# Performance work log

Measured on AMD Instinct MI355X. Metric: run time of the kernel, lower is better.

Reference implementation:

```python
import jax, jax.numpy as jnp
import numpy as np

B, N, K, C, NH = 2, 16384, 16, 256, 4
HD = C // NH  # head_dim = 64


def knn_gather(feat, idx):
    # feat: [B, N, D], idx: [B, N, K] -> [B, N, K, D]
    b, n, k = idx.shape
    d = feat.shape[-1]
    flat = jnp.take_along_axis(feat, idx.reshape(b, n * k)[..., None], axis=1)
    return flat.reshape(b, n, k, d)


def setup_inputs() -> dict:
    key = jax.random.key(0)
    ks = jax.random.split(key, 16)
    s_c = 1.0 / np.sqrt(C)
    s_4 = 1.0 / np.sqrt(4.0)
    s_hd = 1.0 / np.sqrt(HD)
    return {
        'h': jax.random.normal(ks[0], (B, N, C), jnp.float32),
        'P': jax.random.normal(ks[1], (B, 3, N), jnp.float32),
        'idx': jax.random.randint(ks[2], (B, N, K), 0, N),
        'Wq': jax.random.normal(ks[3], (C, C), jnp.float32) * s_c,
        'Wk': jax.random.normal(ks[4], (C, C), jnp.float32) * s_c,
        'Wv': jax.random.normal(ks[5], (C, C), jnp.float32) * s_c,
        'Wp1': jax.random.normal(ks[6], (4, C), jnp.float32) * s_4,
        'bp1': jnp.zeros((C,), jnp.float32),
        'Wp2': jax.random.normal(ks[7], (C, C), jnp.float32) * s_c,
        'bp2': jnp.zeros((C,), jnp.float32),
        'Wa1': jax.random.normal(ks[8], (HD, HD), jnp.float32) * s_hd,
        'ba1': jnp.zeros((HD,), jnp.float32),
        'Wa2': jax.random.normal(ks[9], (HD, 1), jnp.float32) * s_hd,
        'ba2': jnp.zeros((1,), jnp.float32),
        'Wo': jax.random.normal(ks[10], (C, C), jnp.float32) * s_c,
        'bo': jnp.zeros((C,), jnp.float32),
    }


def reference(h, P, idx, Wq, Wk, Wv, Wp1, bp1, Wp2, bp2, Wa1, ba1, Wa2, ba2, Wo, bo):
    b, n, c = h.shape
    P_t = jnp.swapaxes(P, 1, 2)                       # [B, N, 3]
    P_nbr = knn_gather(P_t, idx)                      # [B, N, K, 3]
    rel_pos = P_nbr - P_t[:, :, None, :]              # [B, N, K, 3]
    dist = jnp.linalg.norm(rel_pos, axis=-1, keepdims=True)
    geom = jnp.concatenate([rel_pos, dist], axis=-1)  # [B, N, K, 4]
    pe = jax.nn.relu(geom @ Wp1 + bp1) @ Wp2 + bp2    # [B, N, K, C]
    pe = pe.reshape(b, n, K, NH, HD)

    Q = (h @ Wq).reshape(b, n, 1, NH, HD)
    K_nbr = knn_gather(h @ Wk, idx).reshape(b, n, K, NH, HD)
    V_nbr = knn_gather(h @ Wv, idx).reshape(b, n, K, NH, HD)

    relation = Q - K_nbr + pe                          # [B, N, K, NH, HD]
    logits = jax.nn.relu(relation @ Wa1 + ba1) @ Wa2 + ba2  # [B, N, K, NH, 1]
    attn = jax.nn.softmax(logits, axis=2)              # softmax over K
    agg = jnp.sum(attn * (V_nbr + pe), axis=2)         # [B, N, NH, HD]
    agg = agg.reshape(b, n, c)
    return agg @ Wo + bo
```

## Files before the change

### kernel.cpp

```cpp
#include <hip/hip_runtime.h>
#include <hip/hip_bf16.h>

#define BB 2
#define NN 16384
#define KK 16
#define CC 256
#define NHH 4
#define HDD 64
#define BN (BB*NN)
#define HP 260

typedef __attribute__((ext_vector_type(8))) short short8;
typedef __attribute__((ext_vector_type(4))) short s4;
typedef __attribute__((ext_vector_type(4))) float f32x4;

__device__ __forceinline__ float bf2f(unsigned short u) {
    union { unsigned u32; float f; } x; x.u32 = ((unsigned)u) << 16; return x.f;
}
__device__ __forceinline__ unsigned short f2bf(float f) {
    union { float f; unsigned u; } x; x.f = f;
    unsigned r = x.u + 0x7FFFu + ((x.u >> 16) & 1u);
    return (unsigned short)(r >> 16);
}
__device__ __forceinline__ short8 ld8_lds(const unsigned short* p) {
    s4 lo = *(const s4*)(p);
    s4 hi = *(const s4*)(p + 4);
    short8 r;
    r[0] = lo[0]; r[1] = lo[1]; r[2] = lo[2]; r[3] = lo[3];
    r[4] = hi[0]; r[5] = hi[1]; r[6] = hi[2]; r[7] = hi[3];
    return r;
}

__global__ __launch_bounds__(256) void prep_kernel(
    const float* __restrict__ Wq, const float* __restrict__ Wk,
    const float* __restrict__ Wv, const float* __restrict__ Wp2,
    const float* __restrict__ Wo, const float* __restrict__ Wa1,
    const float* __restrict__ bp2, const float* __restrict__ ba1,
    const float* __restrict__ Wp1,
    unsigned short* WqaT, unsigned short* WkaT, unsigned short* WvT,
    unsigned short* WpeaT, unsigned short* Wp2T, unsigned short* WoT,
    float* b_u, unsigned short* Wp1aT)
{
    const int z = blockIdx.y;
    const int t = threadIdx.x;
    if (z < 3) {
        const float* W = (z == 0) ? Wq : (z == 1) ? Wk : Wp2;
        unsigned short* out = (z == 0) ? WqaT : (z == 1) ? WkaT : WpeaT;
        const int k = blockIdx.x;
        __shared__ float wrow[CC];
        __shared__ float a1[HDD * HDD];
        wrow[t] = W[k * CC + t];
        for (int i = t; i < HDD * HDD; i += 256) a1[i] = Wa1[i];
        __syncthreads();
        const int c = t;
        const int h0 = c & ~63;
        const int cl = c & 63;
        float s = 0.f;
        #pragma unroll 8
        for (int j = 0; j < HDD; ++j) s += wrow[h0 + j] * a1[j * HDD + cl];
        out[c * CC + k] = f2bf(s);
    } else if (z < 6) {
        const float* W = (z == 3) ? Wv : (z == 4) ? Wp2 : Wo;
        unsigned short* out = (z == 3) ? WvT : (z == 4) ? Wp2T : WoT;
        const int k = blockIdx.x;
        out[t * CC + k] = f2bf(W[k * CC + t]);
    } else {
        if (blockIdx.x == 0) {
            __shared__ float a1[HDD * HDD];
            for (int i = t; i < HDD * HDD; i += 256) a1[i] = Wa1[i];
            __syncthreads();
            const int c = t;
            const int h0 = c & ~63;
            const int cl = c & 63;
            float s = ba1[cl];
            #pragma unroll 8
            for (int j = 0; j < HDD; ++j) s += bp2[h0 + j] * a1[j * HDD + cl];
            b_u[c] = s;
        } else if (blockIdx.x == 1) {
            const int c = t;
            #pragma unroll
            for (int j = 0; j < 8; ++j)
                Wp1aT[c * 8 + j] = (j < 4) ? f2bf(Wp1[j * CC + c]) : (unsigned short)0;
        }
    }
}

__global__ __launch_bounds__(256) void h2bf_kernel(const float* __restrict__ h,
                                                   unsigned short* __restrict__ hbf)
{
    const int i = blockIdx.x * blockDim.x + threadIdx.x;
    const float4 v = ((const float4*)h)[i];
    ushort4 o;
    o.x = f2bf(v.x); o.y = f2bf(v.y); o.z = f2bf(v.z); o.w = f2bf(v.w);
    ((ushort4*)hbf)[i] = o;
}

template<bool FINAL>
__global__ __launch_bounds__(256) void gemm64_kernel(
    const unsigned short* __restrict__ A,
    const unsigned short* __restrict__ BT0, const unsigned short* __restrict__ BT1,
    const unsigned short* __restrict__ BT2,
    unsigned short* D0, unsigned short* D1, unsigned short* D2,
    float* Dout, const float* __restrict__ bias)
{
    const int m0 = blockIdx.x * 64;
    const unsigned short* BT;
    unsigned short* Dst = nullptr;
    if (!FINAL) {
        const int z = blockIdx.y;
        BT  = (z == 0) ? BT0 : (z == 1) ? BT1 : BT2;
        Dst = (z == 0) ? D0  : (z == 1) ? D1  : D2;
    } else {
        BT = BT0;
    }

    __shared__ __align__(16) unsigned short As[64 * 264];
    const int t = threadIdx.x;
    #pragma unroll
    for (int i = 0; i < 8; ++i) {
        const int flat = i * 2048 + t * 8;
        const int r = flat >> 8, c = flat & 255;
        short8 v = *(const short8*)(A + (size_t)(m0 + r) * CC + c);
        *(short8*)(&As[r * 264 + c]) = v;
    }
    __syncthreads();

    const int lane = t & 63, w = t >> 6;
    const int lr = lane & 15, lg = lane >> 4;

    f32x4 acc[4][4];
    #pragma unroll
    for (int mi = 0; mi < 4; ++mi)
        #pragma unroll
        for (int ni = 0; ni < 4; ++ni) acc[mi][ni] = (f32x4){0.f, 0.f, 0.f, 0.f};

    #pragma unroll
    for (int kk = 0; kk < 8; ++kk) {
        const int ko = kk * 32 + lg * 8;
        short8 a[4];
        #pragma unroll
        for (int mi = 0; mi < 4; ++mi)
            a[mi] = *(const short8*)(&As[(mi * 16 + lr) * 264 + ko]);
        #pragma unroll
        for (int ni = 0; ni < 4; ++ni) {
            const int col = w * 64 + ni * 16 + lr;
            short8 b = *(const short8*)(BT + (size_t)col * CC + ko);
            #pragma unroll
            for (int mi = 0; mi < 4; ++mi)
                acc[mi][ni] = __builtin_amdgcn_mfma_f32_16x16x32_bf16(a[mi], b, acc[mi][ni], 0, 0, 0);
        }
    }

    #pragma unroll
    for (int mi = 0; mi < 4; ++mi) {
        #pragma unroll
        for (int ni = 0; ni < 4; ++ni) {
            const int col = w * 64 + ni * 16 + lr;
            #pragma unroll
            for (int reg = 0; reg < 4; ++reg) {
                const int row = m0 + mi * 16 + lg * 4 + reg;
                const float v = acc[mi][ni][reg];
                if (FINAL) Dout[(size_t)row * CC + col] = v + bias[col];
                else       Dst[(size_t)row * CC + col] = f2bf(v);
            }
        }
    }
}

__global__ __launch_bounds__(256, 4) void fused_attn_kernel(
    const float* __restrict__ P, const int* __restrict__ idx,
    const unsigned short* __restrict__ Wp1aT, const float* __restrict__ bp1,
    const float* __restrict__ Wa2, const float* __restrict__ bp2,
    const unsigned short* __restrict__ QAbf, const unsigned short* __restrict__ KAbf,
    const unsigned short* __restrict__ Vbf,  const unsigned short* __restrict__ WpeaT,
    const unsigned short* __restrict__ Wp2T, const float* __restrict__ b_u,
    unsigned short* __restrict__ aggbf)
{
    const int pt0 = blockIdx.x * 4;
    const int b = pt0 >> 14;
    const int n0 = pt0 & (NN - 1);
    const int t = threadIdx.x;
    const int lane = t & 63, w = t >> 6;
    const int lr = lane & 15, lg = lane >> 4;

    __shared__ int nbrL[64];
    __shared__ __align__(16) unsigned short geomP[64 * 8];
    __shared__ __align__(16) unsigned short hidL[64 * HP];
    __shared__ __align__(16) unsigned short attnA[16 * 72];
    __shared__ unsigned short vbarL[16 * 72];

    const short8 zero8 = {0, 0, 0, 0, 0, 0, 0, 0};

    float qab[4][4];
    float wa2v[4], bp1v[4];
    #pragma unroll
    for (int ni = 0; ni < 4; ++ni) {
        const int c = w * 64 + ni * 16 + lr;
        wa2v[ni] = Wa2[ni * 16 + lr];
        bp1v[ni] = bp1[c];
        const float bu = b_u[c];
        #pragma unroll
        for (int mi = 0; mi < 4; ++mi)
            qab[mi][ni] = bf2f(QAbf[(size_t)(pt0 + mi) * CC + c]) + bu;
    }

    for (int i = t; i < 576; i += 256) ((unsigned*)attnA)[i] = 0;
    if (t < 64) {
        const int g = t >> 4, k = t & 15;
        const int nb = idx[(size_t)(pt0 + g) * KK + k];
        nbrL[t] = nb;
        const float* Pb = P + (size_t)b * 3 * NN;
        const int nc = n0 + g;
        const float rx = Pb[nb] - Pb[nc];
        const float ry = Pb[NN + nb] - Pb[NN + nc];
        const float rz = Pb[2 * NN + nb] - Pb[2 * NN + nc];
        const float d = sqrtf(rx * rx + ry * ry + rz * rz);
        short8 gp = {(short)f2bf(rx), (short)f2bf(ry), (short)f2bf(rz), (short)f2bf(d),
                     0, 0, 0, 0};
        *(short8*)(&geomP[t * 8]) = gp;
    }
    __syncthreads();

    {
        short8 bb[4];
        #pragma unroll
        for (int ni = 0; ni < 4; ++ni) {
            const int col = w * 64 + ni * 16 + lr;
            bb[ni] = (lg == 0) ? *(const short8*)(Wp1aT + col * 8) : zero8;
        }
        #pragma unroll
        for (int mi = 0; mi < 4; ++mi) {
            short8 ag = (lg == 0) ? *(const short8*)(&geomP[(mi * 16 + lr) * 8]) : zero8;
            #pragma unroll
            for (int ni = 0; ni < 4; ++ni) {
                f32x4 ah = (f32x4){bp1v[ni], bp1v[ni], bp1v[ni], bp1v[ni]};
                ah = __builtin_amdgcn_mfma_f32_16x16x32_bf16(ag, bb[ni], ah, 0, 0, 0);
                const int col = w * 64 + ni * 16 + lr;
                #pragma unroll
                for (int reg = 0; reg < 4; ++reg)
                    hidL[(mi * 16 + lg * 4 + reg) * HP + col] = f2bf(fmaxf(ah[reg], 0.f));
            }
        }
    }
    __syncthreads();

    f32x4 acc[4][4];
    #pragma unroll
    for (int mi = 0; mi < 4; ++mi)
        #pragma unroll
        for (int ni = 0; ni < 4; ++ni) {
            const float v = qab[mi][ni];
            acc[mi][ni] = (f32x4){v, v, v, v};
        }

    #pragma unroll
    for (int kk = 0; kk < 8; ++kk) {
        const int ko = kk * 32 + lg * 8;
        short8 a[4];
        #pragma unroll
        for (int mi = 0; mi < 4; ++mi)
            a[mi] = ld8_lds(&hidL[(mi * 16 + lr) * HP + ko]);
        #pragma unroll
        for (int ni = 0; ni < 4; ++ni) {
            const int col = w * 64 + ni * 16 + lr;
            short8 bfr = *(const short8*)(WpeaT + (size_t)col * CC + ko);
            #pragma unroll
            for (int mi = 0; mi < 4; ++mi)
                acc[mi][ni] = __builtin_amdgcn_mfma_f32_16x16x32_bf16(a[mi], bfr, acc[mi][ni], 0, 0, 0);
        }
    }

    #pragma unroll
    for (int mi = 0; mi < 4; ++mi) {
        unsigned short ka[4][4];
        #pragma unroll
        for (int reg = 0; reg < 4; ++reg) {
            const int r = mi * 16 + lg * 4 + reg;
            const size_t base = ((size_t)b * NN + nbrL[r]) * CC;
            #pragma unroll
            for (int ni = 0; ni < 4; ++ni)
                ka[reg][ni] = KAbf[base + w * 64 + ni * 16 + lr];
        }
        float pl[4];
        #pragma unroll
        for (int reg = 0; reg < 4; ++reg) {
            float s = 0.f;
            #pragma unroll
            for (int ni = 0; ni < 4; ++ni) {
                const float u = acc[mi][ni][reg] - bf2f(ka[reg][ni]);
                s += fmaxf(u, 0.f) * wa2v[ni];
            }
            s += __shfl_xor(s, 1);
            s += __shfl_xor(s, 2);
            s += __shfl_xor(s, 4);
            s += __shfl_xor(s, 8);
            pl[reg] = s;
        }
        float m = fmaxf(fmaxf(pl[0], pl[1]), fmaxf(pl[2], pl[3]));
        m = fmaxf(m, __shfl_xor(m, 16));
        m = fmaxf(m, __shfl_xor(m, 32));
        float e[4], s = 0.f;
        #pragma unroll
        for (int reg = 0; reg < 4; ++reg) { e[reg] = __expf(pl[reg] - m); s += e[reg]; }
        s += __shfl_xor(s, 16);
        s += __shfl_xor(s, 32);
        const float inv = 1.f / s;
        if (lr == 0) {
            #pragma unroll
            for (int reg = 0; reg < 4; ++reg)
                attnA[(mi * 4 + w) * 72 + mi * 16 + lg * 4 + reg] = f2bf(e[reg] * inv);
        }
    }
    __syncthreads();

    unsigned short vv[4][16];
    #pragma unroll
    for (int i = 0; i < 4; ++i) {
        const int gh = w * 4 + i;
        const int g = gh >> 2, hh = gh & 3;
        #pragma unroll
        for (int k = 0; k < 16; ++k) {
            const int r = g * 16 + k;
            vv[i][k] = Vbf[((size_t)b * NN + nbrL[r]) * CC + hh * 64 + lane];
        }
    }

    #pragma unroll
    for (int ni = 0; ni < 4; ++ni) {
        const int colAbs = w * 64 + ni * 16 + lr;
        f32x4 ab = (f32x4){0.f, 0.f, 0.f, 0.f};
        #pragma unroll
        for (int kk = 0; kk < 2; ++kk) {
            short8 aa = ld8_lds(&attnA[lr * 72 + kk * 32 + lg * 8]);
            short8 hb;
            #pragma unroll
            for (int j = 0; j < 8; ++j)
                hb[j] = (short)hidL[(kk * 32 + lg * 8 + j) * HP + colAbs];
            ab = __builtin_amdgcn_mfma_f32_16x16x32_bf16(aa, hb, ab, 0, 0, 0);
        }
        #pragma unroll
        for (int reg = 0; reg < 4; ++reg)
            hidL[(lg * 4 + reg) * HP + colAbs] = f2bf(ab[reg]);
    }

    {
        #pragma unroll
        for (int i = 0; i < 4; ++i) {
            const int gh = w * 4 + i;
            const int g = gh >> 2;
            float s = 0.f;
            #pragma unroll
            for (int k = 0; k < 16; ++k)
                s += bf2f(attnA[gh * 72 + g * 16 + k]) * bf2f(vv[i][k]);
            vbarL[gh * 72 + lane] = f2bf(s);
        }
    }
    __syncthreads();

    f32x4 acc2[4];
    #pragma unroll
    for (int ni = 0; ni < 4; ++ni) acc2[ni] = (f32x4){0.f, 0.f, 0.f, 0.f};
    #pragma unroll
    for (int kk = 0; kk < 8; ++kk) {
        const int ko = kk * 32 + lg * 8;
        short8 a = ld8_lds(&hidL[lr * HP + ko]);
        #pragma unroll
        for (int ni = 0; ni < 4; ++ni) {
            const int col = w * 64 + ni * 16 + lr;
            short8 bfr = *(const short8*)(Wp2T + (size_t)col * CC + ko);
            acc2[ni] = __builtin_amdgcn_mfma_f32_16x16x32_bf16(a, bfr, acc2[ni], 0, 0, 0);
        }
    }
    #pragma unroll
    for (int ni = 0; ni < 4; ++ni) {
        const int cl = ni * 16 + lr;
        const int c = w * 64 + cl;
        float pv;
        if      (w == 0) pv = acc2[ni][0];
        else if (w == 1) pv = acc2[ni][1];
        else if (w == 2) pv = acc2[ni][2];
        else             pv = acc2[ni][3];
        const float v = pv + bf2f(vbarL[(lg * 4 + w) * 72 + cl]) + bp2[c];
        aggbf[(size_t)(pt0 + lg) * CC + c] = f2bf(v);
    }
}

extern "C" void kernel_launch(void* const* d_in, const int* in_sizes, int n_in,
                              void* d_out, int out_size, void* d_ws, size_t ws_size,
                              hipStream_t stream)
{
    const float* h   = (const float*)d_in[0];
    const float* P   = (const float*)d_in[1];
    const int*   idx = (const int*)d_in[2];
    const float* Wq  = (const float*)d_in[3];
    const float* Wk  = (const float*)d_in[4];
    const float* Wv  = (const float*)d_in[5];
    const float* Wp1 = (const float*)d_in[6];
    const float* bp1 = (const float*)d_in[7];
    const float* Wp2 = (const float*)d_in[8];
    const float* bp2 = (const float*)d_in[9];
    const float* Wa1 = (const float*)d_in[10];
    const float* ba1 = (const float*)d_in[11];
    const float* Wa2 = (const float*)d_in[12];
    const float* Wo  = (const float*)d_in[14];
    const float* bo  = (const float*)d_in[15];

    char* ws = (char*)d_ws;
    const size_t MB16 = 16777216;
    unsigned short* WqaT  = (unsigned short*)(ws + 0);
    unsigned short* WkaT  = (unsigned short*)(ws + 131072);
    unsigned short* WvT   = (unsigned short*)(ws + 262144);
    unsigned short* WpeaT = (unsigned short*)(ws + 393216);
    unsigned short* Wp2T  = (unsigned short*)(ws + 524288);
    unsigned short* WoT   = (unsigned short*)(ws + 655360);
    float*          b_u   = (float*)(ws + 786432);
    unsigned short* Wp1aT = (unsigned short*)(ws + 787456);
    const size_t base = 1 << 20;
    unsigned short* hbf   = (unsigned short*)(ws + base + 0 * MB16);
    unsigned short* QAbf  = (unsigned short*)(ws + base + 1 * MB16);
    unsigned short* KAbf  = (unsigned short*)(ws + base + 2 * MB16);
    unsigned short* Vbf   = (unsigned short*)(ws + base + 3 * MB16);
    unsigned short* aggbf = (unsigned short*)(ws + base + 4 * MB16);
    if (ws_size < base + 5 * MB16) return;

    prep_kernel<<<dim3(256, 7), 256, 0, stream>>>(Wq, Wk, Wv, Wp2, Wo, Wa1, bp2, ba1, Wp1,
                                                  WqaT, WkaT, WvT, WpeaT, Wp2T, WoT,
                                                  b_u, Wp1aT);
    h2bf_kernel<<<BN * CC / 4 / 256, 256, 0, stream>>>(h, hbf);
    gemm64_kernel<false><<<dim3(BN / 64, 3), 256, 0, stream>>>(
        hbf, WqaT, WkaT, WvT, QAbf, KAbf, Vbf, nullptr, nullptr);
    fused_attn_kernel<<<BN / 4, 256, 0, stream>>>(P, idx, Wp1aT, bp1, Wa2, bp2,
                                                  QAbf, KAbf, Vbf, WpeaT, Wp2T, b_u, aggbf);
    gemm64_kernel<true><<<dim3(BN / 64, 1), 256, 0, stream>>>(
        aggbf, WoT, nullptr, nullptr, nullptr, nullptr, nullptr, (float*)d_out, bo);
}
```

Before: 395.8 us.

## Fuse bf16 conversion into QKV GEMM, interleave K/V rows, fold bias into Q

The separate h-to-bf16 kernel is removed, and the QKV GEMM now reads fp32 h directly and converts it while staging into LDS. K and V outputs are written interleaved into a single 512-wide row buffer, so each gathered neighbor's K and V values sit in the same row and can share cache lines. The b_u bias add moves from the attention kernel into the Q GEMM epilogue. Together these remove one launch and a full bf16 write/read round trip, and should improve gather locality. The cost is that every z-slice of the GEMM now reads fp32 h, doubling A-load bytes per block, and Q is rounded to bf16 after the bias add.

```diff
diff --git a/kernel.cpp b/kernel.cpp
--- a/kernel.cpp
+++ b/kernel.cpp
@@ -9,6 +9,7 @@
 #define HDD 64
 #define BN (BB*NN)
 #define HP 260
+#define KVP 512
 
 typedef __attribute__((ext_vector_type(8))) short short8;
 typedef __attribute__((ext_vector_type(4))) short s4;
@@ -85,31 +86,20 @@
     }
 }
 
-__global__ __launch_bounds__(256) void h2bf_kernel(const float* __restrict__ h,
-                                                   unsigned short* __restrict__ hbf)
-{
-    const int i = blockIdx.x * blockDim.x + threadIdx.x;
-    const float4 v = ((const float4*)h)[i];
-    ushort4 o;
-    o.x = f2bf(v.x); o.y = f2bf(v.y); o.z = f2bf(v.z); o.w = f2bf(v.w);
-    ((ushort4*)hbf)[i] = o;
-}
-
-template<bool FINAL>
+template<bool FINAL, bool AF32>
 __global__ __launch_bounds__(256) void gemm64_kernel(
-    const unsigned short* __restrict__ A,
+    const void* __restrict__ Asrc,
     const unsigned short* __restrict__ BT0, const unsigned short* __restrict__ BT1,
     const unsigned short* __restrict__ BT2,
-    unsigned short* D0, unsigned short* D1, unsigned short* D2,
+    unsigned short* QA, unsigned short* KV,
     float* Dout, const float* __restrict__ bias)
 {
     const int m0 = blockIdx.x * 64;
     const unsigned short* BT;
-    unsigned short* Dst = nullptr;
+    int z = 0;
     if (!FINAL) {
-        const int z = blockIdx.y;
-        BT  = (z == 0) ? BT0 : (z == 1) ? BT1 : BT2;
-        Dst = (z == 0) ? D0  : (z == 1) ? D1  : D2;
+        z = blockIdx.y;
+        BT = (z == 0) ? BT0 : (z == 1) ? BT1 : BT2;
     } else {
         BT = BT0;
     }
@@ -120,8 +110,20 @@
     for (int i = 0; i < 8; ++i) {
         const int flat = i * 2048 + t * 8;
         const int r = flat >> 8, c = flat & 255;
-        short8 v = *(const short8*)(A + (size_t)(m0 + r) * CC + c);
-        *(short8*)(&As[r * 264 + c]) = v;
+        if (AF32) {
+            const float* Af = (const float*)Asrc;
+            const float4 v0 = *(const float4*)(Af + (size_t)(m0 + r) * CC + c);
+            const float4 v1 = *(const float4*)(Af + (size_t)(m0 + r) * CC + c + 4);
+            short8 v;
+            v[0] = (short)f2bf(v0.x); v[1] = (short)f2bf(v0.y);
+            v[2] = (short)f2bf(v0.z); v[3] = (short)f2bf(v0.w);
+            v[4] = (short)f2bf(v1.x); v[5] = (short)f2bf(v1.y);
+            v[6] = (short)f2bf(v1.z); v[7] = (short)f2bf(v1.w);
+            *(short8*)(&As[r * 264 + c]) = v;
+        } else {
+            short8 v = *(const short8*)((const unsigned short*)Asrc + (size_t)(m0 + r) * CC + c);
+            *(short8*)(&As[r * 264 + c]) = v;
+        }
     }
     __syncthreads();
 
@@ -156,12 +158,18 @@
         #pragma unroll
         for (int ni = 0; ni < 4; ++ni) {
             const int col = w * 64 + ni * 16 + lr;
+            const float bc = (FINAL || z == 0) ? bias[col] : 0.f;
             #pragma unroll
             for (int reg = 0; reg < 4; ++reg) {
                 const int row = m0 + mi * 16 + lg * 4 + reg;
                 const float v = acc[mi][ni][reg];
-                if (FINAL) Dout[(size_t)row * CC + col] = v + bias[col];
-                else       Dst[(size_t)row * CC + col] = f2bf(v);
+                if (FINAL) {
+                    Dout[(size_t)row * CC + col] = v + bias[col];
+                } else if (z == 0) {
+                    QA[(size_t)row * CC + col] = f2bf(v + bc);
+                } else {
+                    KV[(size_t)row * KVP + (z == 1 ? 0 : 256) + col] = f2bf(v);
+                }
             }
         }
     }
@@ -171,9 +179,8 @@
     const float* __restrict__ P, const int* __restrict__ idx,
     const unsigned short* __restrict__ Wp1aT, const float* __restrict__ bp1,
     const float* __restrict__ Wa2, const float* __restrict__ bp2,
-    const unsigned short* __restrict__ QAbf, const unsigned short* __restrict__ KAbf,
-    const unsigned short* __restrict__ Vbf,  const unsigned short* __restrict__ WpeaT,
-    const unsigned short* __restrict__ Wp2T, const float* __restrict__ b_u,
+    const unsigned short* __restrict__ QAbf, const unsigned short* __restrict__ KVbf,
+    const unsigned short* __restrict__ WpeaT, const unsigned short* __restrict__ Wp2T,
     unsigned short* __restrict__ aggbf)
 {
     const int pt0 = blockIdx.x * 4;
@@ -198,10 +205,9 @@
         const int c = w * 64 + ni * 16 + lr;
         wa2v[ni] = Wa2[ni * 16 + lr];
         bp1v[ni] = bp1[c];
-        const float bu = b_u[c];
         #pragma unroll
         for (int mi = 0; mi < 4; ++mi)
-            qab[mi][ni] = bf2f(QAbf[(size_t)(pt0 + mi) * CC + c]) + bu;
+            qab[mi][ni] = bf2f(QAbf[(size_t)(pt0 + mi) * CC + c]);
     }
 
     for (int i = t; i < 576; i += 256) ((unsigned*)attnA)[i] = 0;
@@ -276,10 +282,10 @@
         #pragma unroll
         for (int reg = 0; reg < 4; ++reg) {
             const int r = mi * 16 + lg * 4 + reg;
-            const size_t base = ((size_t)b * NN + nbrL[r]) * CC;
+            const size_t base = ((size_t)b * NN + nbrL[r]) * KVP;
             #pragma unroll
             for (int ni = 0; ni < 4; ++ni)
-                ka[reg][ni] = KAbf[base + w * 64 + ni * 16 + lr];
+                ka[reg][ni] = KVbf[base + w * 64 + ni * 16 + lr];
         }
         float pl[4];
         #pragma unroll
@@ -313,6 +319,7 @@
     }
     __syncthreads();
 
+    const size_t bNN = (size_t)b * NN;
     unsigned short vv[4][16];
     #pragma unroll
     for (int i = 0; i < 4; ++i) {
@@ -321,7 +328,7 @@
         #pragma unroll
         for (int k = 0; k < 16; ++k) {
             const int r = g * 16 + k;
-            vv[i][k] = Vbf[((size_t)b * NN + nbrL[r]) * CC + hh * 64 + lane];
+            vv[i][k] = KVbf[(bNN + nbrL[r]) * KVP + 256 + hh * 64 + lane];
         }
     }
 
@@ -416,21 +423,18 @@
     float*          b_u   = (float*)(ws + 786432);
     unsigned short* Wp1aT = (unsigned short*)(ws + 787456);
     const size_t base = 1 << 20;
-    unsigned short* hbf   = (unsigned short*)(ws + base + 0 * MB16);
-    unsigned short* QAbf  = (unsigned short*)(ws + base + 1 * MB16);
-    unsigned short* KAbf  = (unsigned short*)(ws + base + 2 * MB16);
-    unsigned short* Vbf   = (unsigned short*)(ws + base + 3 * MB16);
-    unsigned short* aggbf = (unsigned short*)(ws + base + 4 * MB16);
-    if (ws_size < base + 5 * MB16) return;
+    unsigned short* QAbf  = (unsigned short*)(ws + base + 0 * MB16);
+    unsigned short* KVbf  = (unsigned short*)(ws + base + 1 * MB16);
+    unsigned short* aggbf = (unsigned short*)(ws + base + 3 * MB16);
+    if (ws_size < base + 4 * MB16) return;
 
     prep_kernel<<<dim3(256, 7), 256, 0, stream>>>(Wq, Wk, Wv, Wp2, Wo, Wa1, bp2, ba1, Wp1,
                                                   WqaT, WkaT, WvT, WpeaT, Wp2T, WoT,
                                                   b_u, Wp1aT);
-    h2bf_kernel<<<BN * CC / 4 / 256, 256, 0, stream>>>(h, hbf);
-    gemm64_kernel<false><<<dim3(BN / 64, 3), 256, 0, stream>>>(
-        hbf, WqaT, WkaT, WvT, QAbf, KAbf, Vbf, nullptr, nullptr);
+    gemm64_kernel<false, true><<<dim3(BN / 64, 3), 256, 0, stream>>>(
+        h, WqaT, WkaT, WvT, QAbf, KVbf, nullptr, b_u);
     fused_attn_kernel<<<BN / 4, 256, 0, stream>>>(P, idx, Wp1aT, bp1, Wa2, bp2,
-                                                  QAbf, KAbf, Vbf, WpeaT, Wp2T, b_u, aggbf);
-    gemm64_kernel<true><<<dim3(BN / 64, 1), 256, 0, stream>>>(
-        aggbf, WoT, nullptr, nullptr, nullptr, nullptr, nullptr, (float*)d_out, bo);
-}
+                                                  QAbf, KVbf, WpeaT, Wp2T, aggbf);
+    gemm64_kernel<true, false><<<dim3(BN / 64, 1), 256, 0, stream>>>(
+        aggbf, WoT, nullptr, nullptr, nullptr, nullptr, (float*)d_out, bo);
+}
```

Result: no change. 395.1 us, median of 2 (-0.2%).
